# Kernel tuning notes

Measured on AMD Instinct MI355X. Metric: run time of the kernel, lower is better.

## Reference

```python
import jax, jax.numpy as jnp
import numpy as np

N = 300000
IN_C = 64
OUT_C = 128
N_Z = 8
B, H, W = 4, 256, 256


def setup_inputs() -> dict:
    key = jax.random.key(0)
    k = jax.random.split(key, 7)
    std = 1.0 / np.sqrt(IN_C)
    return {
        "features": jax.random.normal(k[0], (N, IN_C), dtype=jnp.float32),
        "kernel": jax.random.uniform(k[1], (N_Z, IN_C, OUT_C), dtype=jnp.float32, minval=-std, maxval=std),
        "bias": jnp.zeros((1, OUT_C), dtype=jnp.float32),
        "batch_idx": jax.random.randint(k[2], (N,), 0, B, dtype=jnp.int32),
        "d0_idx": jax.random.randint(k[3], (N,), 0, H, dtype=jnp.int32),
        "d1_idx": jax.random.randint(k[4], (N,), 0, W, dtype=jnp.int32),
        "z_idx": jax.random.randint(k[5], (N,), 0, N_Z, dtype=jnp.int32),
    }


def reference(features, kernel, bias, batch_idx, d0_idx, d1_idx, z_idx):
    # stride s = 1 on the drcv path, so //s is identity
    z = jnp.clip(z_idx, 0, N_Z - 1)
    flat_bev = batch_idx * (H * W) + d0_idx * W + d1_idx  # [N]
    # per-point learned matmul: features[n] @ kernel[z[n]]
    # (computed as a small fixed loop over n_z height bins to avoid
    #  materializing the [N, in_c, out_c] gathered kernel)
    bev_feat = jnp.zeros((features.shape[0], OUT_C), dtype=features.dtype)
    for zz in range(N_Z):
        bev_feat = bev_feat + jnp.where((z == zz)[:, None], features @ kernel[zz], 0.0)
    bev_feat = bev_feat + bias
    # scatter_add into dense BEV
    bev = jnp.zeros((B * H * W, OUT_C), dtype=features.dtype).at[flat_bev].add(bev_feat)
    return bev.reshape(B, H, W, OUT_C).transpose(0, 3, 1, 2)
```

## Files before the change

### kernel.cpp

```cpp
#include <hip/hip_runtime.h>

#define PPB   128
#define NZ    8
#define INC   64
#define OUTC  128
#define NB    4
#define HH    256
#define WWD   256
#define HWD   (HH * WWD)
#define NSEG  (NB * HH)
#define NCELL (NB * HH * WWD)

typedef __attribute__((ext_vector_type(8))) short bf16x8;
typedef __attribute__((ext_vector_type(4))) float f32x4;

__device__ __forceinline__ unsigned bf16_rne(float x) {
    unsigned u = __float_as_uint(x);
    return (u + 0x7FFFu + ((u >> 16) & 1u)) >> 16;
}
__device__ __forceinline__ unsigned pack2(float lo, float hi) {
    return bf16_rne(lo) | (bf16_rne(hi) << 16);
}

__global__ __launch_bounds__(256) void wprep_kernel(const float* __restrict__ kw,
                                                    unsigned short* __restrict__ wt) {
    int z = blockIdx.x;
    const float* src = kw + (size_t)z * INC * OUTC;
    unsigned short* dst = wt + (size_t)z * OUTC * INC;
    int t = threadIdx.x;
    for (int c = t; c < OUTC; c += 256) {
#pragma unroll
        for (int k = 0; k < INC; k += 2) {
            float a = src[(size_t)k * OUTC + c];
            float b = src[(size_t)(k + 1) * OUTC + c];
            *(unsigned*)&dst[(size_t)c * INC + k] = pack2(a, b);
        }
    }
}

__global__ void hist_kernel(const int* __restrict__ z_idx, const int* __restrict__ batch_idx,
                            const int* __restrict__ d0_idx, const int* __restrict__ d1_idx,
                            int* __restrict__ counts, int* __restrict__ cellhist, int n) {
    __shared__ int lc[NZ];
    int t = threadIdx.x;
    if (t < NZ) lc[t] = 0;
    __syncthreads();
    int i = blockIdx.x * blockDim.x + t;
    if (i < n) {
        int z = z_idx[i]; z = z < 0 ? 0 : (z > NZ - 1 ? NZ - 1 : z);
        atomicAdd(&lc[z], 1);
        int cell = (batch_idx[i] * HH + d0_idx[i]) * WWD + d1_idx[i];
        atomicAdd(&cellhist[cell], 1);
    }
    __syncthreads();
    if (t < NZ && lc[t] > 0) atomicAdd(&counts[t], lc[t]);
}

__global__ __launch_bounds__(256) void scan_local(const int* __restrict__ cellhist,
                                                  int* __restrict__ cellstart,
                                                  int* __restrict__ chunksum) {
    __shared__ int ts[256];
    int t = threadIdx.x;
    int base = blockIdx.x * 1024 + t * 4;
    int4 v = *(const int4*)&cellhist[base];
    int s = v.x + v.y + v.z + v.w;
    ts[t] = s;
    __syncthreads();
    for (int d = 1; d < 256; d <<= 1) {
        int x = (t >= d) ? ts[t - d] : 0;
        __syncthreads();
        ts[t] += x;
        __syncthreads();
    }
    int excl = ts[t] - s;
    int4 o;
    o.x = excl; o.y = excl + v.x; o.z = o.y + v.y; o.w = o.z + v.z;
    *(int4*)&cellstart[base] = o;
    if (t == 255) chunksum[blockIdx.x] = ts[255];
}

__global__ __launch_bounds__(256) void scan_top(int* __restrict__ chunksum,
                                                const int* __restrict__ counts,
                                                int* __restrict__ pstart) {
    __shared__ int ts[256];
    int t = threadIdx.x;
    if (t == 0) {
        int off = 0;
        for (int z = 0; z < NZ; ++z) {
            pstart[z] = off;
            off += ((counts[z] + PPB - 1) / PPB) * PPB;
        }
        pstart[NZ] = off;
    }
    int s = chunksum[t];
    ts[t] = s;
    __syncthreads();
    for (int d = 1; d < 256; d <<= 1) {
        int x = (t >= d) ? ts[t - d] : 0;
        __syncthreads();
        ts[t] += x;
        __syncthreads();
    }
    chunksum[t] = ts[t] - s;
}

__global__ __launch_bounds__(256) void scan_add(int* __restrict__ cellstart,
                                                const int* __restrict__ chunksum) {
    int off = chunksum[blockIdx.x];
    if (off == 0) return;
    int base = blockIdx.x * 1024 + threadIdx.x * 4;
    int4 v = *(int4*)&cellstart[base];
    v.x += off; v.y += off; v.z += off; v.w += off;
    *(int4*)&cellstart[base] = v;
}

__global__ void pad_kernel(const int* __restrict__ counts, const int* __restrict__ pstart,
                           int* __restrict__ bins, int* __restrict__ segpos) {
    int z = blockIdx.x;
    int cnt = counts[z];
    int s0 = pstart[z];
    int padded = pstart[z + 1] - s0;
    for (int i = cnt + threadIdx.x; i < padded; i += blockDim.x) {
        bins[s0 + i] = -1;
        segpos[s0 + i] = 0;
    }
}

__global__ void scatter_kernel(const int* __restrict__ z_idx, const int* __restrict__ batch_idx,
                               const int* __restrict__ d0_idx, const int* __restrict__ d1_idx,
                               const int* __restrict__ pstart, int* __restrict__ cursors,
                               int* __restrict__ cellstart,
                               int* __restrict__ bins, int* __restrict__ segpos, int n) {
    __shared__ int lc[NZ];
    __shared__ int lbase[NZ];
    int t = threadIdx.x;
    if (t < NZ) lc[t] = 0;
    __syncthreads();
    int i = blockIdx.x * blockDim.x + t;
    int z = 0, rank = 0;
    bool valid = (i < n);
    if (valid) {
        z = z_idx[i]; z = z < 0 ? 0 : (z > NZ - 1 ? NZ - 1 : z);
        rank = atomicAdd(&lc[z], 1);
    }
    __syncthreads();
    if (t < NZ) lbase[t] = (lc[t] > 0) ? atomicAdd(&cursors[t], lc[t]) : 0;
    __syncthreads();
    if (valid) {
        int slot = pstart[z] + lbase[z] + rank;
        bins[slot] = i;
        int cell = (batch_idx[i] * HH + d0_idx[i]) * WWD + d1_idx[i];
        int r2 = atomicAdd(&cellstart[cell], 1);
        segpos[slot] = 1 + r2;
    }
}

__global__ __launch_bounds__(256) void gemm_kernel(
        const float* __restrict__ features, const unsigned short* __restrict__ wt,
        const float* __restrict__ bias,
        const int* __restrict__ pstart, const int* __restrict__ bins,
        const int* __restrict__ segpos, unsigned* __restrict__ bevf) {
    __shared__ __align__(16) char lbuf[32768];
    __shared__ int psl[PPB];
    char* Abf = lbuf;
    char* Wbf = lbuf + 16384;

    int start = blockIdx.x * PPB;
    int total = pstart[NZ];
    if (start >= total) return;
    int z = 0;
#pragma unroll
    for (int zz = 1; zz < NZ; ++zz)
        if (start >= pstart[zz]) z = zz;

    int tid = threadIdx.x;
    if (tid < PPB) psl[tid] = segpos[start + tid];

    {
        int r = tid >> 1, half = tid & 1;
        int raw = bins[start + r];
        int nid = raw < 0 ? 0 : raw;
        const float4* fp = (const float4*)(features + (size_t)nid * INC) + half * 8;
        float4 f[8];
#pragma unroll
        for (int q = 0; q < 8; ++q) f[q] = fp[q];
        unsigned u[16];
#pragma unroll
        for (int m = 0; m < 8; ++m) {
            u[2 * m]     = pack2(f[m].x, f[m].y);
            u[2 * m + 1] = pack2(f[m].z, f[m].w);
        }
#pragma unroll
        for (int ch = 0; ch < 4; ++ch) {
            int off = (r * 128 + half * 64 + ch * 16) ^ ((r & 7) << 4);
            uint4 val = make_uint4(u[4 * ch], u[4 * ch + 1], u[4 * ch + 2], u[4 * ch + 3]);
            *(uint4*)(Abf + off) = val;
        }
    }
    {
        const uint4* src = (const uint4*)(wt + (size_t)z * OUTC * INC);
#pragma unroll
        for (int i = 0; i < 4; ++i) {
            int s = tid + 256 * i;
            int c = s >> 3, ch = s & 7;
            int off = (c * 128 + ch * 16) ^ ((c & 7) << 4);
            *(uint4*)(Wbf + off) = src[s];
        }
    }
    __syncthreads();

    int wv_ = tid >> 6, l = tid & 63;
    int wr = wv_ >> 1, wc = wv_ & 1;

    f32x4 acc[4][4];
#pragma unroll
    for (int i = 0; i < 4; ++i)
#pragma unroll
        for (int j = 0; j < 4; ++j) acc[i][j] = (f32x4){0.f, 0.f, 0.f, 0.f};

#pragma unroll
    for (int kc = 0; kc < 2; ++kc) {
        bf16x8 af[4], bfr[4];
#pragma unroll
        for (int pb = 0; pb < 4; ++pb) {
            int p = wr * 64 + pb * 16 + (l & 15);
            int off = (p * 128 + kc * 64 + (l >> 4) * 16) ^ ((p & 7) << 4);
            af[pb] = *(const bf16x8*)(Abf + off);
        }
#pragma unroll
        for (int cb = 0; cb < 4; ++cb) {
            int c = wc * 64 + cb * 16 + (l & 15);
            int off = (c * 128 + kc * 64 + (l >> 4) * 16) ^ ((c & 7) << 4);
            bfr[cb] = *(const bf16x8*)(Wbf + off);
        }
#pragma unroll
        for (int pb = 0; pb < 4; ++pb)
#pragma unroll
            for (int cb = 0; cb < 4; ++cb)
                acc[pb][cb] = __builtin_amdgcn_mfma_f32_16x16x32_bf16(
                    af[pb], bfr[cb], acc[pb][cb], 0, 0, 0);
    }
    __syncthreads();

    float bias_c[4];
#pragma unroll
    for (int cb = 0; cb < 4; ++cb) bias_c[cb] = bias[wc * 64 + cb * 16 + (l & 15)];

#pragma unroll
    for (int pb = 0; pb < 4; ++pb) {
#pragma unroll
        for (int cb = 0; cb < 4; ++cb) {
            int c = wc * 64 + cb * 16 + (l & 15);
#pragma unroll
            for (int q = 0; q < 4; ++q) {
                int prow = wr * 64 + pb * 16 + (l >> 4) * 4 + q;
                float v = acc[pb][cb][q] + bias_c[cb];
                int byteoff = (prow * 256 + c * 2) ^ (((prow >> 2) & 3) << 5);
                *(unsigned short*)(lbuf + byteoff) = (unsigned short)bf16_rne(v);
            }
        }
    }
    __syncthreads();

#pragma unroll
    for (int j = 0; j < 8; ++j) {
        int s = j * 256 + tid;
        int prow = s >> 4, chunk = s & 15;
        int byteoff = (prow * 256 + chunk * 16) ^ (((prow >> 2) & 3) << 5);
        uint4 val = *(const uint4*)(lbuf + byteoff);
        int pos = psl[prow];
        *((uint4*)(bevf + (size_t)pos * 64) + chunk) = val;
    }
}

__global__ __launch_bounds__(512) void reduce_kernel(
        const unsigned* __restrict__ bevf, const int* __restrict__ cellstart,
        float* __restrict__ out) {
    __shared__ unsigned tile[256 * 64];
    int t = threadIdx.x;
    int blk = blockIdx.x;
    blk = (blk & 7) * (NSEG / 8) + (blk >> 3);
    int seg = blk;
    int wv = t >> 6, l = t & 63;

    int cell0 = seg * WWD + wv * 32;
    int idx = cell0 + l - 1;
    int bound = 0;
    if (l <= 32) bound = (idx < 0) ? 0 : cellstart[idx];
    int r0 = __shfl(bound, 0);
    int r1 = __shfl(bound, 32);

    int j = 0;
    int ce = __shfl(bound, 1);
    float f0 = 0.f, f1 = 0.f;
    for (int r = r0; r < r1; r += 4) {
        unsigned v[4];
#pragma unroll
        for (int u = 0; u < 4; ++u) {
            int rr = (r + u < r1) ? r + u : r1 - 1;
            v[u] = bevf[(size_t)(rr + 1) * 64 + l];
        }
#pragma unroll
        for (int u = 0; u < 4; ++u) {
            if (r + u >= r1) break;
            while (r + u >= ce) {
                int w = wv * 32 + j;
                tile[w * 64 + ((l + w) & 63)] = pack2(f0, f1);
                f0 = 0.f; f1 = 0.f;
                ++j;
                ce = __shfl(bound, j + 1);
            }
            f0 += __uint_as_float(v[u] << 16);
            f1 += __uint_as_float(v[u] & 0xFFFF0000u);
        }
    }
    while (j < 32) {
        int w = wv * 32 + j;
        tile[w * 64 + ((l + w) & 63)] = pack2(f0, f1);
        f0 = 0.f; f1 = 0.f;
        ++j;
    }
    __syncthreads();

    int b = seg >> 8, h = seg & 255;
    float* ob = out + (size_t)b * OUTC * HWD + (size_t)h * WWD;
#pragma unroll
    for (int r = 0; r < 16; ++r) {
        int c = wv + 8 * r;
        int d = c >> 1;
        float* op = ob + (size_t)c * HWD;
#pragma unroll
        for (int q = 0; q < 4; ++q) {
            int w = 64 * q + l;
            unsigned v = tile[w * 64 + ((d + w) & 63)];
            op[w] = __uint_as_float((c & 1) ? (v & 0xFFFF0000u) : (v << 16));
        }
    }
}

__global__ __launch_bounds__(256) void naive_kernel(
        const float* __restrict__ features, const float* __restrict__ kw,
        const float* __restrict__ bias,
        const int* __restrict__ bidx, const int* __restrict__ d0,
        const int* __restrict__ d1, const int* __restrict__ zi,
        float* __restrict__ out, int n) {
    long long gid = (long long)blockIdx.x * blockDim.x + threadIdx.x;
    int pid = (int)(gid >> 7);
    int c   = (int)(gid & (OUTC - 1));
    if (pid >= n) return;
    int z = zi[pid]; z = z < 0 ? 0 : (z > NZ - 1 ? NZ - 1 : z);
    const float4* fp = (const float4*)(features + (size_t)pid * INC);
    const float* wp = kw + (size_t)z * INC * OUTC + c;
    float a0 = bias[c], a1 = 0.f, a2 = 0.f, a3 = 0.f;
#pragma unroll
    for (int i = 0; i < INC / 4; ++i) {
        float4 f = fp[i];
        a0 += f.x * wp[(size_t)(4 * i + 0) * OUTC];
        a1 += f.y * wp[(size_t)(4 * i + 1) * OUTC];
        a2 += f.z * wp[(size_t)(4 * i + 2) * OUTC];
        a3 += f.w * wp[(size_t)(4 * i + 3) * OUTC];
    }
    float acc = (a0 + a1) + (a2 + a3);
    size_t oidx = ((size_t)bidx[pid] * OUTC + c) * HWD + (size_t)d0[pid] * WWD + d1[pid];
    unsafeAtomicAdd(&out[oidx], acc);
}

extern "C" void kernel_launch(void* const* d_in, const int* in_sizes, int n_in,
                              void* d_out, int out_size, void* d_ws, size_t ws_size,
                              hipStream_t stream) {
    const float* features = (const float*)d_in[0];
    const float* kw       = (const float*)d_in[1];
    const float* bias     = (const float*)d_in[2];
    const int* batch_idx  = (const int*)d_in[3];
    const int* d0_idx     = (const int*)d_in[4];
    const int* d1_idx     = (const int*)d_in[5];
    const int* z_idx      = (const int*)d_in[6];
    float* out = (float*)d_out;
    int n = in_sizes[0] / INC;

    size_t binsElems = (size_t)n + (size_t)NZ * PPB;
    size_t bevfBytes = (binsElems + 1) * OUTC * 2;
    size_t wtOff     = (bevfBytes + 255) & ~(size_t)255;
    size_t metaOff   = wtOff + (size_t)NZ * OUTC * INC * 2;
    size_t chOff     = (metaOff + 32 * 4 + 255) & ~(size_t)255;
    size_t csOff     = chOff + (size_t)NCELL * 4;
    size_t ckOff     = csOff + (size_t)(NCELL + 4) * 4;
    size_t binsOff   = (ckOff + 256 * 4 + 255) & ~(size_t)255;
    size_t posOff    = binsOff + binsElems * 4;
    size_t need      = posOff + binsElems * 4 + 16;

    if (ws_size >= need) {
        char* ws = (char*)d_ws;
        unsigned* bevf = (unsigned*)ws;
        unsigned short* wt = (unsigned short*)(ws + wtOff);
        int* meta      = (int*)(ws + metaOff);
        int* counts    = meta;
        int* cursors   = meta + 8;
        int* pstart    = meta + 16;
        int* cellhist  = (int*)(ws + chOff);
        int* cellstart = (int*)(ws + csOff);
        int* chunksum  = (int*)(ws + ckOff);
        int* bins      = (int*)(ws + binsOff);
        int* segpos    = (int*)(ws + posOff);

        hipMemsetAsync(meta, 0, 32 * 4, stream);
        hipMemsetAsync(cellhist, 0, (size_t)NCELL * 4, stream);

        int gb = (n + 255) / 256;
        wprep_kernel<<<NZ, 256, 0, stream>>>(kw, wt);
        hist_kernel<<<gb, 256, 0, stream>>>(z_idx, batch_idx, d0_idx, d1_idx,
                                            counts, cellhist, n);
        scan_local<<<256, 256, 0, stream>>>(cellhist, cellstart, chunksum);
        scan_top<<<1, 256, 0, stream>>>(chunksum, counts, pstart);
        scan_add<<<256, 256, 0, stream>>>(cellstart, chunksum);
        pad_kernel<<<NZ, 128, 0, stream>>>(counts, pstart, bins, segpos);
        scatter_kernel<<<gb, 256, 0, stream>>>(z_idx, batch_idx, d0_idx, d1_idx,
                                               pstart, cursors, cellstart,
                                               bins, segpos, n);

        int nblk = (int)((binsElems + PPB - 1) / PPB) + 1;
        gemm_kernel<<<nblk, 256, 0, stream>>>(features, wt, bias, pstart, bins,
                                              segpos, bevf);

        reduce_kernel<<<NSEG, 512, 0, stream>>>(bevf, cellstart, out);
    } else {
        hipMemsetAsync(out, 0, (size_t)out_size * sizeof(float), stream);
        long long threads = (long long)n * OUTC;
        int gb = (int)((threads + 255) / 256);
        naive_kernel<<<gb, 256, 0, stream>>>(features, kw, bias, batch_idx, d0_idx,
                                             d1_idx, z_idx, out, n);
    }
}
```

Measured before the change: 154.5 us.

## Merge scan kernels, drop pad kernel, and vectorize reduce output stores

Moves the pstart computation into scan_local and replaces scan_top and scan_add with one kernel in which each block reduces its own prefix of chunk sums, so two launches go away. The pad kernel is removed; the GEMM now masks rows past each bin's count and reads counts directly. The reduce kernel's tile swizzle changes so each lane writes four consecutive output columns as a float4 store instead of four scalar stores. The trade-off is a redundant 256-element reduction in every scan_add2 block. The GEMM still writes padded rows with segpos 0, which relies on slot 0 of bevf being a dummy.

```diff
diff --git a/kernel.cpp b/kernel.cpp
--- a/kernel.cpp
+++ b/kernel.cpp
@@ -58,7 +58,17 @@
 
 __global__ __launch_bounds__(256) void scan_local(const int* __restrict__ cellhist,
                                                   int* __restrict__ cellstart,
-                                                  int* __restrict__ chunksum) {
+                                                  int* __restrict__ chunksum,
+                                                  const int* __restrict__ counts,
+                                                  int* __restrict__ pstart) {
+    if (blockIdx.x == 0 && threadIdx.x == 0) {
+        int off = 0;
+        for (int z = 0; z < NZ; ++z) {
+            pstart[z] = off;
+            off += ((counts[z] + PPB - 1) / PPB) * PPB;
+        }
+        pstart[NZ] = off;
+    }
     __shared__ int ts[256];
     int t = threadIdx.x;
     int base = blockIdx.x * 1024 + t * 4;
@@ -79,51 +89,23 @@
     if (t == 255) chunksum[blockIdx.x] = ts[255];
 }
 
-__global__ __launch_bounds__(256) void scan_top(int* __restrict__ chunksum,
-                                                const int* __restrict__ counts,
-                                                int* __restrict__ pstart) {
+__global__ __launch_bounds__(256) void scan_add2(int* __restrict__ cellstart,
+                                                 const int* __restrict__ chunksum) {
     __shared__ int ts[256];
     int t = threadIdx.x;
-    if (t == 0) {
-        int off = 0;
-        for (int z = 0; z < NZ; ++z) {
-            pstart[z] = off;
-            off += ((counts[z] + PPB - 1) / PPB) * PPB;
-        }
-        pstart[NZ] = off;
-    }
-    int s = chunksum[t];
-    ts[t] = s;
-    __syncthreads();
-    for (int d = 1; d < 256; d <<= 1) {
-        int x = (t >= d) ? ts[t - d] : 0;
+    int b = blockIdx.x;
+    ts[t] = (t < b) ? chunksum[t] : 0;
+    __syncthreads();
+    for (int d = 128; d > 0; d >>= 1) {
+        if (t < d) ts[t] += ts[t + d];
         __syncthreads();
-        ts[t] += x;
-        __syncthreads();
-    }
-    chunksum[t] = ts[t] - s;
-}
-
-__global__ __launch_bounds__(256) void scan_add(int* __restrict__ cellstart,
-                                                const int* __restrict__ chunksum) {
-    int off = chunksum[blockIdx.x];
+    }
+    int off = ts[0];
     if (off == 0) return;
-    int base = blockIdx.x * 1024 + threadIdx.x * 4;
+    int base = b * 1024 + t * 4;
     int4 v = *(int4*)&cellstart[base];
     v.x += off; v.y += off; v.z += off; v.w += off;
     *(int4*)&cellstart[base] = v;
-}
-
-__global__ void pad_kernel(const int* __restrict__ counts, const int* __restrict__ pstart,
-                           int* __restrict__ bins, int* __restrict__ segpos) {
-    int z = blockIdx.x;
-    int cnt = counts[z];
-    int s0 = pstart[z];
-    int padded = pstart[z + 1] - s0;
-    for (int i = cnt + threadIdx.x; i < padded; i += blockDim.x) {
-        bins[s0 + i] = -1;
-        segpos[s0 + i] = 0;
-    }
 }
 
 __global__ void scatter_kernel(const int* __restrict__ z_idx, const int* __restrict__ batch_idx,
@@ -157,7 +139,7 @@
 
 __global__ __launch_bounds__(256) void gemm_kernel(
         const float* __restrict__ features, const unsigned short* __restrict__ wt,
-        const float* __restrict__ bias,
+        const float* __restrict__ bias, const int* __restrict__ counts,
         const int* __restrict__ pstart, const int* __restrict__ bins,
         const int* __restrict__ segpos, unsigned* __restrict__ bevf) {
     __shared__ __align__(16) char lbuf[32768];
@@ -172,13 +154,15 @@
 #pragma unroll
     for (int zz = 1; zz < NZ; ++zz)
         if (start >= pstart[zz]) z = zz;
+    int limit = pstart[z] + counts[z] - start;
+    if (limit <= 0) return;
 
     int tid = threadIdx.x;
-    if (tid < PPB) psl[tid] = segpos[start + tid];
+    if (tid < PPB) psl[tid] = (tid < limit) ? segpos[start + tid] : 0;
 
     {
         int r = tid >> 1, half = tid & 1;
-        int raw = bins[start + r];
+        int raw = (r < limit) ? bins[start + r] : 0;
         int nid = raw < 0 ? 0 : raw;
         const float4* fp = (const float4*)(features + (size_t)nid * INC) + half * 8;
         float4 f[8];
@@ -305,7 +289,7 @@
             if (r + u >= r1) break;
             while (r + u >= ce) {
                 int w = wv * 32 + j;
-                tile[w * 64 + ((l + w) & 63)] = pack2(f0, f1);
+                tile[w * 64 + ((l + w + (w >> 2)) & 63)] = pack2(f0, f1);
                 f0 = 0.f; f1 = 0.f;
                 ++j;
                 ce = __shfl(bound, j + 1);
@@ -316,7 +300,7 @@
     }
     while (j < 32) {
         int w = wv * 32 + j;
-        tile[w * 64 + ((l + w) & 63)] = pack2(f0, f1);
+        tile[w * 64 + ((l + w + (w >> 2)) & 63)] = pack2(f0, f1);
         f0 = 0.f; f1 = 0.f;
         ++j;
     }
@@ -328,13 +312,17 @@
     for (int r = 0; r < 16; ++r) {
         int c = wv + 8 * r;
         int d = c >> 1;
-        float* op = ob + (size_t)c * HWD;
-#pragma unroll
-        for (int q = 0; q < 4; ++q) {
-            int w = 64 * q + l;
-            unsigned v = tile[w * 64 + ((d + w) & 63)];
-            op[w] = __uint_as_float((c & 1) ? (v & 0xFFFF0000u) : (v << 16));
-        }
+        bool hi = c & 1;
+        unsigned v0 = tile[(4 * l + 0) * 64 + ((d + 5 * l + 0) & 63)];
+        unsigned v1 = tile[(4 * l + 1) * 64 + ((d + 5 * l + 1) & 63)];
+        unsigned v2 = tile[(4 * l + 2) * 64 + ((d + 5 * l + 2) & 63)];
+        unsigned v3 = tile[(4 * l + 3) * 64 + ((d + 5 * l + 3) & 63)];
+        float4 o;
+        o.x = __uint_as_float(hi ? (v0 & 0xFFFF0000u) : (v0 << 16));
+        o.y = __uint_as_float(hi ? (v1 & 0xFFFF0000u) : (v1 << 16));
+        o.z = __uint_as_float(hi ? (v2 & 0xFFFF0000u) : (v2 << 16));
+        o.w = __uint_as_float(hi ? (v3 & 0xFFFF0000u) : (v3 << 16));
+        *(float4*)(ob + (size_t)c * HWD + 4 * l) = o;
     }
 }
 
@@ -410,17 +398,16 @@
         wprep_kernel<<<NZ, 256, 0, stream>>>(kw, wt);
         hist_kernel<<<gb, 256, 0, stream>>>(z_idx, batch_idx, d0_idx, d1_idx,
                                             counts, cellhist, n);
-        scan_local<<<256, 256, 0, stream>>>(cellhist, cellstart, chunksum);
-        scan_top<<<1, 256, 0, stream>>>(chunksum, counts, pstart);
-        scan_add<<<256, 256, 0, stream>>>(cellstart, chunksum);
-        pad_kernel<<<NZ, 128, 0, stream>>>(counts, pstart, bins, segpos);
+        scan_local<<<256, 256, 0, stream>>>(cellhist, cellstart, chunksum,
+                                            counts, pstart);
+        scan_add2<<<256, 256, 0, stream>>>(cellstart, chunksum);
         scatter_kernel<<<gb, 256, 0, stream>>>(z_idx, batch_idx, d0_idx, d1_idx,
                                                pstart, cursors, cellstart,
                                                bins, segpos, n);
 
         int nblk = (int)((binsElems + PPB - 1) / PPB) + 1;
-        gemm_kernel<<<nblk, 256, 0, stream>>>(features, wt, bias, pstart, bins,
-                                              segpos, bevf);
+        gemm_kernel<<<nblk, 256, 0, stream>>>(features, wt, bias, counts, pstart,
+                                              bins, segpos, bevf);
 
         reduce_kernel<<<NSEG, 512, 0, stream>>>(bevf, cellstart, out);
     } else {
```

Result: no change. 152.5 us (-1.3%).
